# Kernel optimization log

Measured on AMD Instinct MI355X. Metric: run time of the kernel, lower is better.

The kernel has to match this reference:

```python
import jax, jax.numpy as jnp
import numpy as np

N_NODES = 50000
N_EDGES = 800000
N_GRAPHS = 256
D_FEAT = 96
HIDDEN = 32


def setup_inputs() -> dict:
    key = jax.random.key(0)
    ks = jax.random.split(key, 8)
    x = jax.random.normal(ks[0], (N_NODES, D_FEAT), dtype=jnp.float32)
    edge_index = jax.random.randint(ks[1], (2, N_EDGES), 0, N_NODES, dtype=jnp.int64)
    batch = jnp.sort(jax.random.randint(ks[2], (N_NODES,), 0, N_GRAPHS, dtype=jnp.int64))
    W1 = jax.random.normal(ks[3], (D_FEAT, HIDDEN), dtype=jnp.float32) * 0.05
    b1 = jnp.zeros((HIDDEN,), dtype=jnp.float32)
    W2 = jax.random.normal(ks[4], (HIDDEN, HIDDEN), dtype=jnp.float32) * 0.05
    b2 = jnp.zeros((HIDDEN,), dtype=jnp.float32)
    Wc = jax.random.normal(ks[5], (HIDDEN, 2), dtype=jnp.float32) * 0.05
    bc = jnp.zeros((2,), dtype=jnp.float32)
    return {"x": x, "edge_index": edge_index, "batch": batch,
            "W1": W1, "b1": b1, "W2": W2, "b2": b2, "Wc": Wc, "bc": bc}


def reference(x, edge_index, batch, W1, b1, W2, b2, Wc, bc):
    src, dst = edge_index[0], edge_index[1]
    # GIN aggregation (eps=0): h_i = x_i + sum_{j -> i} x_j, scatter-add over edges
    agg = jax.ops.segment_sum(x[src], dst, num_segments=N_NODES)
    h = agg + x
    # 2-layer MLP inside GINConv
    h = jnp.maximum(h @ W1 + b1, 0.0) @ W2 + b2
    # outer ReLU (F.relu in forward)
    h = jnp.maximum(h, 0.0)
    # global mean pool per graph
    sums = jax.ops.segment_sum(h, batch, num_segments=N_GRAPHS)          # [G, H]
    counts = jax.ops.segment_sum(jnp.ones((N_NODES,), h.dtype), batch,
                                 num_segments=N_GRAPHS)                   # [G]
    pooled = sums / jnp.maximum(counts, 1.0)[:, None]
    return pooled @ Wc + bc  # [G, 2]
```

## Files before the change

kernel.cpp:

```cpp
#include <hip/hip_runtime.h>
#include <hip/hip_fp16.h>

#define N_NODES 50000
#define N_EDGES 800000
#define N_GRAPHS 256
#define D_FEAT 96
#define HIDDEN 32

#define NB 196
#define PB 400
#define PCHUNK 2000
#define SEGCAP 64
#define GWIN 16
#define LCAP 6400
#define XT 64
#define XBLK 782
#define XS_STRIDE 97
#define DUMMY_NODE N_NODES

__global__ void __launch_bounds__(256)
k_front(const float* __restrict__ x, const float* __restrict__ W1,
        __half* __restrict__ y16,
        const int* __restrict__ src, const int* __restrict__ dst,
        unsigned int* __restrict__ binned, unsigned short* __restrict__ cnt,
        float* __restrict__ sums, float* __restrict__ counts) {
    int blk = blockIdx.x;
    int tid = threadIdx.x;
    if (blk < PB) {
        __shared__ int hcur[NB];
        for (int i = tid; i < NB; i += 256) hcur[i] = 0;
        __syncthreads();

        int e0 = blk * PCHUNK, e1 = e0 + PCHUNK;
        for (int e = e0 + tid; e < e1; e += 256) {
            int sn = src[e];
            int d  = dst[e];
            int b  = d >> 8;
            int pos = atomicAdd(&hcur[b], 1);
            if (pos < SEGCAP)
                binned[((size_t)b * PB + blk) * SEGCAP + pos] =
                    (unsigned)sn | ((unsigned)(d & 255) << 16);
        }
        __syncthreads();

        for (int i = tid; i < NB; i += 256) {
            int c = hcur[i]; if (c > SEGCAP) c = SEGCAP;
            cnt[i * PB + blk] = (unsigned short)c;
        }
    } else {
        __shared__ float xs[XT * XS_STRIDE];
        int xb = blk - PB;
        int n0 = xb * XT;
        int nn = N_NODES - n0; if (nn > XT) nn = XT;

        int gid = xb * 256 + tid;
        if (gid < N_GRAPHS * HIDDEN) sums[gid] = 0.f;
        if (gid < N_GRAPHS) counts[gid] = 0.f;
        if (xb == 0 && tid < HIDDEN)
            y16[(size_t)DUMMY_NODE * HIDDEN + tid] = __float2half(0.f);

        const float4* xsrc = (const float4*)(x + (size_t)n0 * D_FEAT);
        int nf4 = nn * (D_FEAT / 4);
        for (int idx = tid; idx < nf4; idx += 256) {
            int ln = (idx * 2731) >> 16;
            int k4 = idx - ln * 24;
            float4 v = xsrc[idx];
            float* dp = &xs[ln * XS_STRIDE + k4 * 4];
            dp[0] = v.x; dp[1] = v.y; dp[2] = v.z; dp[3] = v.w;
        }
        __syncthreads();

        int lane = tid & 63;
        int f0 = (tid >> 6) << 3;
        f0 = __builtin_amdgcn_readfirstlane(f0);

        if (lane < nn) {
            const float* xr = &xs[lane * XS_STRIDE];
            const float4* W1v = (const float4*)W1;
            float acc[8];
#pragma unroll
            for (int j = 0; j < 8; ++j) acc[j] = 0.f;
#pragma unroll
            for (int k = 0; k < D_FEAT; ++k) {
                float xv = xr[k];
                float4 wa = W1v[k * 8 + (f0 >> 2)];
                float4 wb = W1v[k * 8 + (f0 >> 2) + 1];
                acc[0] = fmaf(xv, wa.x, acc[0]);
                acc[1] = fmaf(xv, wa.y, acc[1]);
                acc[2] = fmaf(xv, wa.z, acc[2]);
                acc[3] = fmaf(xv, wa.w, acc[3]);
                acc[4] = fmaf(xv, wb.x, acc[4]);
                acc[5] = fmaf(xv, wb.y, acc[5]);
                acc[6] = fmaf(xv, wb.z, acc[6]);
                acc[7] = fmaf(xv, wb.w, acc[7]);
            }
            __half2 h01 = __floats2half2_rn(acc[0], acc[1]);
            __half2 h23 = __floats2half2_rn(acc[2], acc[3]);
            __half2 h45 = __floats2half2_rn(acc[4], acc[5]);
            __half2 h67 = __floats2half2_rn(acc[6], acc[7]);
            float4 pack;
            pack.x = __uint_as_float(*(const unsigned*)&h01);
            pack.y = __uint_as_float(*(const unsigned*)&h23);
            pack.z = __uint_as_float(*(const unsigned*)&h45);
            pack.w = __uint_as_float(*(const unsigned*)&h67);
            *(float4*)&y16[(size_t)(n0 + lane) * HIDDEN + f0] = pack;
        }
    }
}

__global__ void __launch_bounds__(1024)
k_agg(const unsigned int* __restrict__ binned, const unsigned short* __restrict__ cnt,
      const __half* __restrict__ y16, const int* __restrict__ batch,
      const float* __restrict__ b1, const float* __restrict__ W2,
      const float* __restrict__ b2,
      float* __restrict__ sums, float* __restrict__ counts) {
    __shared__ unsigned int list[LCAP];
    __shared__ unsigned short list2[LCAP];
    __shared__ unsigned int sA[512], sB[512];
    __shared__ unsigned short cs[PB];
    __shared__ unsigned int sOfs[PB];
    __shared__ unsigned int ncnt[256];
    __shared__ unsigned int offs[257];
    __shared__ unsigned int cur[256];
    __shared__ float w2s[HIDDEN * HIDDEN];
    __shared__ float accs[GWIN * HIDDEN];
    __shared__ float cntsl[GWIN];

    int tid = threadIdx.x;
    int bin = blockIdx.x;
    if (tid < 256) ncnt[tid] = 0;
    for (int i = tid; i < HIDDEN * HIDDEN; i += 1024) w2s[i] = W2[i];
    if (tid < GWIN * HIDDEN) accs[tid] = 0.f;
    if (tid < GWIN) cntsl[tid] = 0.f;
    if (tid < 512) {
        unsigned c = (tid < PB) ? (unsigned)cnt[bin * PB + tid] : 0u;
        if (tid < PB) cs[tid] = (unsigned short)c;
        sA[tid] = c;
    }
    __syncthreads();

    unsigned *ps = sA, *pd = sB;
    for (int d = 1; d < 512; d <<= 1) {
        if (tid < 512) { unsigned v = ps[tid]; if (tid >= d) v += ps[tid - d]; pd[tid] = v; }
        __syncthreads();
        unsigned* t = ps; ps = pd; pd = t;
    }
    if (tid < PB) sOfs[tid] = tid ? ps[tid - 1] : 0u;
    int ecount = (int)ps[PB - 1];
    if (ecount > LCAP) ecount = LCAP;
    __syncthreads();

    const unsigned int* ebase = binned + (size_t)bin * PB * SEGCAP;
    for (int idx = tid; idx < PB * SEGCAP; idx += 1024) {
        int s = idx >> 6;
        int i = idx & 63;
        if (i < (int)cs[s]) {
            unsigned pos = sOfs[s] + i;
            if (pos < LCAP) list[pos] = ebase[idx];
        }
    }
    __syncthreads();

    for (int e = tid; e < ecount; e += 1024)
        atomicAdd(&ncnt[list[e] >> 16], 1u);
    __syncthreads();

    if (tid < 256) sA[tid] = (ncnt[tid] + 7u) & ~7u;
    __syncthreads();
    ps = sA; pd = sB;
    for (int d = 1; d < 256; d <<= 1) {
        if (tid < 256) { unsigned v = ps[tid]; if (tid >= d) v += ps[tid - d]; pd[tid] = v; }
        __syncthreads();
        unsigned* t = ps; ps = pd; pd = t;
    }
    if (tid < 256) {
        offs[tid + 1] = ps[tid];
        cur[tid] = tid ? ps[tid - 1] : 0u;
    }
    if (tid == 0) offs[0] = 0;
    __syncthreads();

    for (int e = tid; e < ecount; e += 1024) {
        unsigned p = list[e];
        unsigned pos = atomicAdd(&cur[p >> 16], 1u);
        if (pos < LCAP) list2[pos] = (unsigned short)(p & 0xFFFFu);
    }
    __syncthreads();
    if (tid < 256) {
        unsigned i0 = cur[tid], i1 = offs[tid + 1];
        for (unsigned i = i0; i < i1 && i < LCAP; ++i)
            list2[i] = (unsigned short)DUMMY_NODE;
    }
    __syncthreads();

    int node0 = bin << 8;
    int nn = N_NODES - node0; if (nn > 256) nn = 256;
    int g = tid >> 5;
    int f = tid & 31;
    int gfirst = batch[node0];

    for (int ln = g * 8; ln < g * 8 + 8; ++ln) {
        if (ln >= nn) break;
        int node = node0 + ln;
        float acc = __half2float(y16[(size_t)node * HIDDEN + f]);
        int j = offs[ln], jend = offs[ln + 1];
        for (; j < jend; j += 8) {
            ushort4 qa = *(const ushort4*)&list2[j];
            ushort4 qb = *(const ushort4*)&list2[j + 4];
            float a0 = __half2float(y16[(size_t)qa.x * HIDDEN + f]);
            float a1 = __half2float(y16[(size_t)qa.y * HIDDEN + f]);
            float a2 = __half2float(y16[(size_t)qa.z * HIDDEN + f]);
            float a3 = __half2float(y16[(size_t)qa.w * HIDDEN + f]);
            float a4 = __half2float(y16[(size_t)qb.x * HIDDEN + f]);
            float a5 = __half2float(y16[(size_t)qb.y * HIDDEN + f]);
            float a6 = __half2float(y16[(size_t)qb.z * HIDDEN + f]);
            float a7 = __half2float(y16[(size_t)qb.w * HIDDEN + f]);
            acc += ((a0 + a1) + (a2 + a3)) + ((a4 + a5) + (a6 + a7));
        }

        float h1 = fmaxf(acc + b1[f], 0.f);
        float h2 = b2[f];
#pragma unroll
        for (int k = 0; k < HIDDEN; ++k)
            h2 = fmaf(__shfl(h1, k, 32), w2s[k * HIDDEN + f], h2);
        float h = fmaxf(h2, 0.f);

        int gr = batch[node];
        int b = gr - gfirst;
        if (b < GWIN) {
            atomicAdd(&accs[b * HIDDEN + f], h);
            if (f == 0) atomicAdd(&cntsl[b], 1.f);
        } else {
            atomicAdd(&sums[(size_t)gr * HIDDEN + f], h);
            if (f == 0) atomicAdd(&counts[gr], 1.f);
        }
    }
    __syncthreads();

    for (int i = tid; i < GWIN * HIDDEN; i += 1024) {
        float v = accs[i];
        if (v != 0.f) atomicAdd(&sums[(size_t)gfirst * HIDDEN + i], v);
    }
    if (tid < GWIN) {
        float c = cntsl[tid];
        if (c != 0.f) atomicAdd(&counts[gfirst + tid], c);
    }
}

__global__ void k_out(const float* __restrict__ sums, const float* __restrict__ counts,
                      const float* __restrict__ Wc, const float* __restrict__ bc,
                      float* __restrict__ out) {
    int g = threadIdx.x;
    if (g >= N_GRAPHS) return;
    float inv = 1.f / fmaxf(counts[g], 1.f);
    float o0 = bc[0], o1 = bc[1];
#pragma unroll
    for (int k = 0; k < HIDDEN; ++k) {
        float p = sums[(size_t)g * HIDDEN + k] * inv;
        o0 = fmaf(p, Wc[k * 2 + 0], o0);
        o1 = fmaf(p, Wc[k * 2 + 1], o1);
    }
    out[g * 2 + 0] = o0;
    out[g * 2 + 1] = o1;
}

extern "C" void kernel_launch(void* const* d_in, const int* in_sizes, int n_in,
                              void* d_out, int out_size, void* d_ws, size_t ws_size,
                              hipStream_t stream) {
    const float* x     = (const float*)d_in[0];
    const int*   ei    = (const int*)d_in[1];
    const int*   batch = (const int*)d_in[2];
    const float* W1    = (const float*)d_in[3];
    const float* b1    = (const float*)d_in[4];
    const float* W2    = (const float*)d_in[5];
    const float* b2    = (const float*)d_in[6];
    const float* Wc    = (const float*)d_in[7];
    const float* bc    = (const float*)d_in[8];
    float* out = (float*)d_out;

    char* ws = (char*)d_ws;
    float*          sums   = (float*)ws;
    float*          counts = (float*)(ws + 32768);
    unsigned short* cnt    = (unsigned short*)(ws + 33792);
    unsigned int*   binned = (unsigned int*)(ws + 190592);
    __half*         y16    = (__half*)(ws + 20260992);

    k_front<<<PB + XBLK, 256, 0, stream>>>(
        x, W1, y16, ei, ei + N_EDGES, binned, cnt, sums, counts);

    k_agg<<<NB, 1024, 0, stream>>>(binned, cnt, y16, batch,
                                   b1, W2, b2, sums, counts);

    k_out<<<1, 256, 0, stream>>>(sums, counts, Wc, bc, out);
}
```

Baseline: 134.6 us.

## Replace in-block CSR build with direct LDS atomic accumulation per destination

```diff
diff --git a/kernel.cpp b/kernel.cpp
--- a/kernel.cpp
+++ b/kernel.cpp
@@ -12,7 +12,6 @@
 #define PCHUNK 2000
 #define SEGCAP 64
 #define GWIN 16
-#define LCAP 6400
 #define XT 64
 #define XBLK 782
 #define XS_STRIDE 97
@@ -114,112 +113,80 @@
       const float* __restrict__ b1, const float* __restrict__ W2,
       const float* __restrict__ b2,
       float* __restrict__ sums, float* __restrict__ counts) {
-    __shared__ unsigned int list[LCAP];
-    __shared__ unsigned short list2[LCAP];
-    __shared__ unsigned int sA[512], sB[512];
+    __shared__ float acc[256 * HIDDEN];
     __shared__ unsigned short cs[PB];
-    __shared__ unsigned int sOfs[PB];
-    __shared__ unsigned int ncnt[256];
-    __shared__ unsigned int offs[257];
-    __shared__ unsigned int cur[256];
     __shared__ float w2s[HIDDEN * HIDDEN];
+    __shared__ float b1s[HIDDEN], b2s[HIDDEN];
     __shared__ float accs[GWIN * HIDDEN];
     __shared__ float cntsl[GWIN];
 
     int tid = threadIdx.x;
     int bin = blockIdx.x;
-    if (tid < 256) ncnt[tid] = 0;
+
+    for (int i = tid; i < 256 * HIDDEN; i += 1024) acc[i] = 0.f;
     for (int i = tid; i < HIDDEN * HIDDEN; i += 1024) w2s[i] = W2[i];
+    if (tid < HIDDEN) { b1s[tid] = b1[tid]; b2s[tid] = b2[tid]; }
     if (tid < GWIN * HIDDEN) accs[tid] = 0.f;
     if (tid < GWIN) cntsl[tid] = 0.f;
-    if (tid < 512) {
-        unsigned c = (tid < PB) ? (unsigned)cnt[bin * PB + tid] : 0u;
-        if (tid < PB) cs[tid] = (unsigned short)c;
-        sA[tid] = c;
-    }
+    if (tid < PB) cs[tid] = cnt[bin * PB + tid];
     __syncthreads();
 
-    unsigned *ps = sA, *pd = sB;
-    for (int d = 1; d < 512; d <<= 1) {
-        if (tid < 512) { unsigned v = ps[tid]; if (tid >= d) v += ps[tid - d]; pd[tid] = v; }
-        __syncthreads();
-        unsigned* t = ps; ps = pd; pd = t;
-    }
-    if (tid < PB) sOfs[tid] = tid ? ps[tid - 1] : 0u;
-    int ecount = (int)ps[PB - 1];
-    if (ecount > LCAP) ecount = LCAP;
-    __syncthreads();
-
+    int g = tid >> 5;
+    int f = tid & 31;
     const unsigned int* ebase = binned + (size_t)bin * PB * SEGCAP;
-    for (int idx = tid; idx < PB * SEGCAP; idx += 1024) {
-        int s = idx >> 6;
-        int i = idx & 63;
-        if (i < (int)cs[s]) {
-            unsigned pos = sOfs[s] + i;
-            if (pos < LCAP) list[pos] = ebase[idx];
-        }
-    }
-    __syncthreads();
-
-    for (int e = tid; e < ecount; e += 1024)
-        atomicAdd(&ncnt[list[e] >> 16], 1u);
-    __syncthreads();
-
-    if (tid < 256) sA[tid] = (ncnt[tid] + 7u) & ~7u;
-    __syncthreads();
-    ps = sA; pd = sB;
-    for (int d = 1; d < 256; d <<= 1) {
-        if (tid < 256) { unsigned v = ps[tid]; if (tid >= d) v += ps[tid - d]; pd[tid] = v; }
-        __syncthreads();
-        unsigned* t = ps; ps = pd; pd = t;
-    }
-    if (tid < 256) {
-        offs[tid + 1] = ps[tid];
-        cur[tid] = tid ? ps[tid - 1] : 0u;
-    }
-    if (tid == 0) offs[0] = 0;
-    __syncthreads();
-
-    for (int e = tid; e < ecount; e += 1024) {
-        unsigned p = list[e];
-        unsigned pos = atomicAdd(&cur[p >> 16], 1u);
-        if (pos < LCAP) list2[pos] = (unsigned short)(p & 0xFFFFu);
-    }
-    __syncthreads();
-    if (tid < 256) {
-        unsigned i0 = cur[tid], i1 = offs[tid + 1];
-        for (unsigned i = i0; i < i1 && i < LCAP; ++i)
-            list2[i] = (unsigned short)DUMMY_NODE;
+
+    for (int s = g; s < PB; s += 32) {
+        int c = (int)cs[s];
+        const unsigned int* seg = ebase + (size_t)s * SEGCAP;
+        unsigned p0 = (f < c) ? seg[f] : (unsigned)DUMMY_NODE;
+        int c0 = c < 32 ? c : 32;
+        int c0r = (c0 + 3) & ~3;
+        for (int i = 0; i < c0r; i += 4) {
+            unsigned pa = __shfl(p0, i,     32);
+            unsigned pb = __shfl(p0, i + 1, 32);
+            unsigned pc = __shfl(p0, i + 2, 32);
+            unsigned pd = __shfl(p0, i + 3, 32);
+            float va = __half2float(y16[(size_t)(pa & 0xFFFFu) * HIDDEN + f]);
+            float vb = __half2float(y16[(size_t)(pb & 0xFFFFu) * HIDDEN + f]);
+            float vc = __half2float(y16[(size_t)(pc & 0xFFFFu) * HIDDEN + f]);
+            float vd = __half2float(y16[(size_t)(pd & 0xFFFFu) * HIDDEN + f]);
+            atomicAdd(&acc[(pa >> 16) * HIDDEN + f], va);
+            atomicAdd(&acc[(pb >> 16) * HIDDEN + f], vb);
+            atomicAdd(&acc[(pc >> 16) * HIDDEN + f], vc);
+            atomicAdd(&acc[(pd >> 16) * HIDDEN + f], vd);
+        }
+        if (c > 32) {
+            unsigned p1 = (f + 32 < c) ? seg[f + 32] : (unsigned)DUMMY_NODE;
+            int c1r = (c - 32 + 3) & ~3;
+            for (int i = 0; i < c1r; i += 4) {
+                unsigned pa = __shfl(p1, i,     32);
+                unsigned pb = __shfl(p1, i + 1, 32);
+                unsigned pc = __shfl(p1, i + 2, 32);
+                unsigned pd = __shfl(p1, i + 3, 32);
+                float va = __half2float(y16[(size_t)(pa & 0xFFFFu) * HIDDEN + f]);
+                float vb = __half2float(y16[(size_t)(pb & 0xFFFFu) * HIDDEN + f]);
+                float vc = __half2float(y16[(size_t)(pc & 0xFFFFu) * HIDDEN + f]);
+                float vd = __half2float(y16[(size_t)(pd & 0xFFFFu) * HIDDEN + f]);
+                atomicAdd(&acc[(pa >> 16) * HIDDEN + f], va);
+                atomicAdd(&acc[(pb >> 16) * HIDDEN + f], vb);
+                atomicAdd(&acc[(pc >> 16) * HIDDEN + f], vc);
+                atomicAdd(&acc[(pd >> 16) * HIDDEN + f], vd);
+            }
+        }
     }
     __syncthreads();
 
     int node0 = bin << 8;
     int nn = N_NODES - node0; if (nn > 256) nn = 256;
-    int g = tid >> 5;
-    int f = tid & 31;
     int gfirst = batch[node0];
 
     for (int ln = g * 8; ln < g * 8 + 8; ++ln) {
         if (ln >= nn) break;
         int node = node0 + ln;
-        float acc = __half2float(y16[(size_t)node * HIDDEN + f]);
-        int j = offs[ln], jend = offs[ln + 1];
-        for (; j < jend; j += 8) {
-            ushort4 qa = *(const ushort4*)&list2[j];
-            ushort4 qb = *(const ushort4*)&list2[j + 4];
-            float a0 = __half2float(y16[(size_t)qa.x * HIDDEN + f]);
-            float a1 = __half2float(y16[(size_t)qa.y * HIDDEN + f]);
-            float a2 = __half2float(y16[(size_t)qa.z * HIDDEN + f]);
-            float a3 = __half2float(y16[(size_t)qa.w * HIDDEN + f]);
-            float a4 = __half2float(y16[(size_t)qb.x * HIDDEN + f]);
-            float a5 = __half2float(y16[(size_t)qb.y * HIDDEN + f]);
-            float a6 = __half2float(y16[(size_t)qb.z * HIDDEN + f]);
-            float a7 = __half2float(y16[(size_t)qb.w * HIDDEN + f]);
-            acc += ((a0 + a1) + (a2 + a3)) + ((a4 + a5) + (a6 + a7));
-        }
-
-        float h1 = fmaxf(acc + b1[f], 0.f);
-        float h2 = b2[f];
+        float a = acc[ln * HIDDEN + f]
+                + __half2float(y16[(size_t)node * HIDDEN + f]);
+        float h1 = fmaxf(a + b1s[f], 0.f);
+        float h2 = b2s[f];
 #pragma unroll
         for (int k = 0; k < HIDDEN; ++k)
             h2 = fmaf(__shfl(h1, k, 32), w2s[k * HIDDEN + f], h2);
```

New measurement: 325.1 us. 2.41x slower.

## Stage binned edges in shared-memory rings and flush 16-entry vector chunks

Applied to the files above, without the earlier changes.

```diff
diff --git a/kernel.cpp b/kernel.cpp
--- a/kernel.cpp
+++ b/kernel.cpp
@@ -24,31 +24,70 @@
         const int* __restrict__ src, const int* __restrict__ dst,
         unsigned int* __restrict__ binned, unsigned short* __restrict__ cnt,
         float* __restrict__ sums, float* __restrict__ counts) {
+    __shared__ __align__(16) char smem[26656];
     int blk = blockIdx.x;
     int tid = threadIdx.x;
     if (blk < PB) {
-        __shared__ int hcur[NB];
-        for (int i = tid; i < NB; i += 256) hcur[i] = 0;
+        unsigned int* q  = (unsigned int*)smem;
+        int* qpos        = (int*)(smem + 25088);
+        int* qflushed    = (int*)(smem + 25088 + 784);
+        for (int i = tid; i < NB; i += 256) { qpos[i] = 0; qflushed[i] = 0; }
         __syncthreads();
 
-        int e0 = blk * PCHUNK, e1 = e0 + PCHUNK;
-        for (int e = e0 + tid; e < e1; e += 256) {
-            int sn = src[e];
-            int d  = dst[e];
-            int b  = d >> 8;
-            int pos = atomicAdd(&hcur[b], 1);
-            if (pos < SEGCAP)
-                binned[((size_t)b * PB + blk) * SEGCAP + pos] =
-                    (unsigned)sn | ((unsigned)(d & 255) << 16);
-        }
-        __syncthreads();
-
-        for (int i = tid; i < NB; i += 256) {
-            int c = hcur[i]; if (c > SEGCAP) c = SEGCAP;
-            cnt[i * PB + blk] = (unsigned short)c;
+        int e0 = blk * PCHUNK;
+        for (int it = 0; it < PCHUNK; it += 256) {
+            int idx = it + tid;
+            if (idx < PCHUNK) {
+                int e  = e0 + idx;
+                int sn = src[e];
+                int d  = dst[e];
+                int b  = d >> 8;
+                unsigned w = (unsigned)sn | ((unsigned)(d & 255) << 16);
+                int pos = atomicAdd(&qpos[b], 1);
+                q[b * 32 + (pos & 31)] = w;
+            }
+            __syncthreads();
+            if (tid < NB) {
+                int p  = qpos[tid];
+                int fl = qflushed[tid];
+                if (fl + 16 <= p && fl + 16 <= SEGCAP) {
+                    unsigned int* qp = q + tid * 32;
+                    do {
+                        int base = fl & 31;
+                        uint4 c0 = *(const uint4*)&qp[base];
+                        uint4 c1 = *(const uint4*)&qp[base + 4];
+                        uint4 c2 = *(const uint4*)&qp[base + 8];
+                        uint4 c3 = *(const uint4*)&qp[base + 12];
+                        uint4* gb = (uint4*)(binned +
+                            ((size_t)tid * PB + blk) * SEGCAP + fl);
+                        gb[0] = c0; gb[1] = c1; gb[2] = c2; gb[3] = c3;
+                        fl += 16;
+                    } while (fl + 16 <= p && fl + 16 <= SEGCAP);
+                    qflushed[tid] = fl;
+                }
+            }
+            __syncthreads();
+        }
+        if (tid < NB) {
+            int p  = qpos[tid];
+            int fl = qflushed[tid];
+            int pcap = p < SEGCAP ? p : SEGCAP;
+            cnt[tid * PB + blk] = (unsigned short)pcap;
+            unsigned int* qp = q + tid * 32;
+            while (fl < pcap) {
+                int base = fl & 31;
+                uint4 c0 = *(const uint4*)&qp[base];
+                uint4 c1 = *(const uint4*)&qp[base + 4];
+                uint4 c2 = *(const uint4*)&qp[base + 8];
+                uint4 c3 = *(const uint4*)&qp[base + 12];
+                uint4* gb = (uint4*)(binned +
+                    ((size_t)tid * PB + blk) * SEGCAP + fl);
+                gb[0] = c0; gb[1] = c1; gb[2] = c2; gb[3] = c3;
+                fl += 16;
+            }
         }
     } else {
-        __shared__ float xs[XT * XS_STRIDE];
+        float* xs = (float*)smem;
         int xb = blk - PB;
         int n0 = xb * XT;
         int nn = N_NODES - n0; if (nn > XT) nn = XT;
```

New measurement: 133.5 us. About the same (-0.9%).

## Split front kernel, vectorize edge binning, prefetch binned edges in aggregation

Applied to the files above, without the earlier changes.

```diff
diff --git a/kernel.cpp b/kernel.cpp
--- a/kernel.cpp
+++ b/kernel.cpp
@@ -8,9 +8,10 @@
 #define HIDDEN 32
 
 #define NB 196
-#define PB 400
-#define PCHUNK 2000
-#define SEGCAP 64
+#define PB 500
+#define PCHUNK 1600
+#define SEGCAP 32
+#define NLOAD 16
 #define GWIN 16
 #define LCAP 6400
 #define XT 64
@@ -19,92 +20,104 @@
 #define DUMMY_NODE N_NODES
 
 __global__ void __launch_bounds__(256)
-k_front(const float* __restrict__ x, const float* __restrict__ W1,
-        __half* __restrict__ y16,
-        const int* __restrict__ src, const int* __restrict__ dst,
-        unsigned int* __restrict__ binned, unsigned short* __restrict__ cnt,
-        float* __restrict__ sums, float* __restrict__ counts) {
+k_part(const int* __restrict__ src, const int* __restrict__ dst,
+       unsigned int* __restrict__ binned, unsigned short* __restrict__ cnt) {
+    __shared__ int hcur[NB];
     int blk = blockIdx.x;
     int tid = threadIdx.x;
-    if (blk < PB) {
-        __shared__ int hcur[NB];
-        for (int i = tid; i < NB; i += 256) hcur[i] = 0;
-        __syncthreads();
-
-        int e0 = blk * PCHUNK, e1 = e0 + PCHUNK;
-        for (int e = e0 + tid; e < e1; e += 256) {
-            int sn = src[e];
-            int d  = dst[e];
-            int b  = d >> 8;
-            int pos = atomicAdd(&hcur[b], 1);
-            if (pos < SEGCAP)
-                binned[((size_t)b * PB + blk) * SEGCAP + pos] =
-                    (unsigned)sn | ((unsigned)(d & 255) << 16);
-        }
-        __syncthreads();
-
-        for (int i = tid; i < NB; i += 256) {
-            int c = hcur[i]; if (c > SEGCAP) c = SEGCAP;
-            cnt[i * PB + blk] = (unsigned short)c;
-        }
-    } else {
-        __shared__ float xs[XT * XS_STRIDE];
-        int xb = blk - PB;
-        int n0 = xb * XT;
-        int nn = N_NODES - n0; if (nn > XT) nn = XT;
-
-        int gid = xb * 256 + tid;
-        if (gid < N_GRAPHS * HIDDEN) sums[gid] = 0.f;
-        if (gid < N_GRAPHS) counts[gid] = 0.f;
-        if (xb == 0 && tid < HIDDEN)
-            y16[(size_t)DUMMY_NODE * HIDDEN + tid] = __float2half(0.f);
-
-        const float4* xsrc = (const float4*)(x + (size_t)n0 * D_FEAT);
-        int nf4 = nn * (D_FEAT / 4);
-        for (int idx = tid; idx < nf4; idx += 256) {
-            int ln = (idx * 2731) >> 16;
-            int k4 = idx - ln * 24;
-            float4 v = xsrc[idx];
-            float* dp = &xs[ln * XS_STRIDE + k4 * 4];
-            dp[0] = v.x; dp[1] = v.y; dp[2] = v.z; dp[3] = v.w;
-        }
-        __syncthreads();
-
-        int lane = tid & 63;
-        int f0 = (tid >> 6) << 3;
-        f0 = __builtin_amdgcn_readfirstlane(f0);
-
-        if (lane < nn) {
-            const float* xr = &xs[lane * XS_STRIDE];
-            const float4* W1v = (const float4*)W1;
-            float acc[8];
-#pragma unroll
-            for (int j = 0; j < 8; ++j) acc[j] = 0.f;
-#pragma unroll
-            for (int k = 0; k < D_FEAT; ++k) {
-                float xv = xr[k];
-                float4 wa = W1v[k * 8 + (f0 >> 2)];
-                float4 wb = W1v[k * 8 + (f0 >> 2) + 1];
-                acc[0] = fmaf(xv, wa.x, acc[0]);
-                acc[1] = fmaf(xv, wa.y, acc[1]);
-                acc[2] = fmaf(xv, wa.z, acc[2]);
-                acc[3] = fmaf(xv, wa.w, acc[3]);
-                acc[4] = fmaf(xv, wb.x, acc[4]);
-                acc[5] = fmaf(xv, wb.y, acc[5]);
-                acc[6] = fmaf(xv, wb.z, acc[6]);
-                acc[7] = fmaf(xv, wb.w, acc[7]);
-            }
-            __half2 h01 = __floats2half2_rn(acc[0], acc[1]);
-            __half2 h23 = __floats2half2_rn(acc[2], acc[3]);
-            __half2 h45 = __floats2half2_rn(acc[4], acc[5]);
-            __half2 h67 = __floats2half2_rn(acc[6], acc[7]);
-            float4 pack;
-            pack.x = __uint_as_float(*(const unsigned*)&h01);
-            pack.y = __uint_as_float(*(const unsigned*)&h23);
-            pack.z = __uint_as_float(*(const unsigned*)&h45);
-            pack.w = __uint_as_float(*(const unsigned*)&h67);
-            *(float4*)&y16[(size_t)(n0 + lane) * HIDDEN + f0] = pack;
-        }
+    for (int i = tid; i < NB; i += 256) hcur[i] = 0;
+    __syncthreads();
+
+    int e0 = blk * PCHUNK, e1 = e0 + PCHUNK;
+    for (int it = 0; it < PCHUNK; it += 1024) {
+        int e = e0 + it + tid * 4;
+        if (e < e1) {
+            int4 s4 = *(const int4*)&src[e];
+            int4 d4 = *(const int4*)&dst[e];
+            unsigned w0 = (unsigned)s4.x | ((unsigned)(d4.x & 255) << 16);
+            unsigned w1 = (unsigned)s4.y | ((unsigned)(d4.y & 255) << 16);
+            unsigned w2 = (unsigned)s4.z | ((unsigned)(d4.z & 255) << 16);
+            unsigned w3 = (unsigned)s4.w | ((unsigned)(d4.w & 255) << 16);
+            int b0 = d4.x >> 8, b1 = d4.y >> 8, b2 = d4.z >> 8, b3 = d4.w >> 8;
+            int p0 = atomicAdd(&hcur[b0], 1);
+            int p1 = atomicAdd(&hcur[b1], 1);
+            int p2 = atomicAdd(&hcur[b2], 1);
+            int p3 = atomicAdd(&hcur[b3], 1);
+            if (p0 < SEGCAP) binned[((size_t)b0 * PB + blk) * SEGCAP + p0] = w0;
+            if (p1 < SEGCAP) binned[((size_t)b1 * PB + blk) * SEGCAP + p1] = w1;
+            if (p2 < SEGCAP) binned[((size_t)b2 * PB + blk) * SEGCAP + p2] = w2;
+            if (p3 < SEGCAP) binned[((size_t)b3 * PB + blk) * SEGCAP + p3] = w3;
+        }
+    }
+    __syncthreads();
+
+    for (int i = tid; i < NB; i += 256) {
+        int c = hcur[i]; if (c > SEGCAP) c = SEGCAP;
+        cnt[i * PB + blk] = (unsigned short)c;
+    }
+}
+
+__global__ void __launch_bounds__(256)
+k_x(const float* __restrict__ x, const float* __restrict__ W1,
+    __half* __restrict__ y16, float* __restrict__ sums,
+    float* __restrict__ counts) {
+    __shared__ float xs[XT * XS_STRIDE];
+    int xb = blockIdx.x;
+    int tid = threadIdx.x;
+    int n0 = xb * XT;
+    int nn = N_NODES - n0; if (nn > XT) nn = XT;
+
+    int gid = xb * 256 + tid;
+    if (gid < N_GRAPHS * HIDDEN) sums[gid] = 0.f;
+    if (gid < N_GRAPHS) counts[gid] = 0.f;
+    if (xb == 0 && tid < HIDDEN)
+        y16[(size_t)DUMMY_NODE * HIDDEN + tid] = __float2half(0.f);
+
+    const float4* xsrc = (const float4*)(x + (size_t)n0 * D_FEAT);
+    int nf4 = nn * (D_FEAT / 4);
+    for (int idx = tid; idx < nf4; idx += 256) {
+        int ln = (idx * 2731) >> 16;
+        int k4 = idx - ln * 24;
+        float4 v = xsrc[idx];
+        float* dp = &xs[ln * XS_STRIDE + k4 * 4];
+        dp[0] = v.x; dp[1] = v.y; dp[2] = v.z; dp[3] = v.w;
+    }
+    __syncthreads();
+
+    int lane = tid & 63;
+    int f0 = (tid >> 6) << 3;
+    f0 = __builtin_amdgcn_readfirstlane(f0);
+
+    if (lane < nn) {
+        const float* xr = &xs[lane * XS_STRIDE];
+        const float4* W1v = (const float4*)W1;
+        float acc[8];
+#pragma unroll
+        for (int j = 0; j < 8; ++j) acc[j] = 0.f;
+#pragma unroll
+        for (int k = 0; k < D_FEAT; ++k) {
+            float xv = xr[k];
+            float4 wa = W1v[k * 8 + (f0 >> 2)];
+            float4 wb = W1v[k * 8 + (f0 >> 2) + 1];
+            acc[0] = fmaf(xv, wa.x, acc[0]);
+            acc[1] = fmaf(xv, wa.y, acc[1]);
+            acc[2] = fmaf(xv, wa.z, acc[2]);
+            acc[3] = fmaf(xv, wa.w, acc[3]);
+            acc[4] = fmaf(xv, wb.x, acc[4]);
+            acc[5] = fmaf(xv, wb.y, acc[5]);
+            acc[6] = fmaf(xv, wb.z, acc[6]);
+            acc[7] = fmaf(xv, wb.w, acc[7]);
+        }
+        __half2 h01 = __floats2half2_rn(acc[0], acc[1]);
+        __half2 h23 = __floats2half2_rn(acc[2], acc[3]);
+        __half2 h45 = __floats2half2_rn(acc[4], acc[5]);
+        __half2 h67 = __floats2half2_rn(acc[6], acc[7]);
+        float4 pack;
+        pack.x = __uint_as_float(*(const unsigned*)&h01);
+        pack.y = __uint_as_float(*(const unsigned*)&h23);
+        pack.z = __uint_as_float(*(const unsigned*)&h45);
+        pack.w = __uint_as_float(*(const unsigned*)&h67);
+        *(float4*)&y16[(size_t)(n0 + lane) * HIDDEN + f0] = pack;
     }
 }
 
@@ -129,7 +142,7 @@
     int tid = threadIdx.x;
     int bin = blockIdx.x;
     if (tid < 256) ncnt[tid] = 0;
-    for (int i = tid; i < HIDDEN * HIDDEN; i += 1024) w2s[i] = W2[i];
+    w2s[tid] = W2[tid];
     if (tid < GWIN * HIDDEN) accs[tid] = 0.f;
     if (tid < GWIN) cntsl[tid] = 0.f;
     if (tid < 512) {
@@ -137,6 +150,12 @@
         if (tid < PB) cs[tid] = (unsigned short)c;
         sA[tid] = c;
     }
+
+    const unsigned int* ebase = binned + (size_t)bin * PB * SEGCAP;
+    unsigned u[NLOAD];
+#pragma unroll
+    for (int j = 0; j < NLOAD; ++j)
+        u[j] = ebase[tid + j * 1024];
     __syncthreads();
 
     unsigned *ps = sA, *pd = sB;
@@ -150,13 +169,16 @@
     if (ecount > LCAP) ecount = LCAP;
     __syncthreads();
 
-    const unsigned int* ebase = binned + (size_t)bin * PB * SEGCAP;
-    for (int idx = tid; idx < PB * SEGCAP; idx += 1024) {
-        int s = idx >> 6;
-        int i = idx & 63;
-        if (i < (int)cs[s]) {
-            unsigned pos = sOfs[s] + i;
-            if (pos < LCAP) list[pos] = ebase[idx];
+#pragma unroll
+    for (int j = 0; j < NLOAD; ++j) {
+        int idx = tid + j * 1024;
+        if (idx < PB * SEGCAP) {
+            int s = idx >> 5;
+            int i = idx & 31;
+            if (i < (int)cs[s]) {
+                unsigned pos = sOfs[s] + i;
+                if (pos < LCAP) list[pos] = u[j];
+            }
         }
     }
     __syncthreads();
@@ -282,11 +304,12 @@
     float*          sums   = (float*)ws;
     float*          counts = (float*)(ws + 32768);
     unsigned short* cnt    = (unsigned short*)(ws + 33792);
-    unsigned int*   binned = (unsigned int*)(ws + 190592);
-    __half*         y16    = (__half*)(ws + 20260992);
-
-    k_front<<<PB + XBLK, 256, 0, stream>>>(
-        x, W1, y16, ei, ei + N_EDGES, binned, cnt, sums, counts);
+    unsigned int*   binned = (unsigned int*)(ws + 230400);
+    __half*         y16    = (__half*)(ws + 12774400);
+
+    k_part<<<PB, 256, 0, stream>>>(ei, ei + N_EDGES, binned, cnt);
+
+    k_x<<<XBLK, 256, 0, stream>>>(x, W1, y16, sums, counts);
 
     k_agg<<<NB, 1024, 0, stream>>>(binned, cnt, y16, batch,
                                    b1, W2, b2, sums, counts);
```

Result: faster. 131.9 us (-2.0%).
